# Kernel tuning notes

Hardware: AMD Instinct MI355X
Metric: run time of the kernel (lower is better)

The kernel has to match this reference:

```python
import jax, jax.numpy as jnp
import numpy as np

B, T, D = 2, 2048, 2048
H, KVH = 16, 4
HD = D // H            # 128
HALF = HD // 2         # 64
EPS = 1e-6


def zc_rmsnorm(x, scale):
    # zero-centred RMSNorm: (1+scale) * x / rms(x), rms in fp32
    rms = jnp.sqrt(jnp.mean(x.astype(jnp.float32) ** 2, axis=-1, keepdims=True) + EPS)
    return ((1.0 + scale) * x / rms).astype(x.dtype)


def apply_rope(x, cos, sin):
    # x: [B, h, T, HD]; cos/sin: [T, HALF]
    t = x.shape[2]
    c = cos[:t][None, None, :, :]
    s = sin[:t][None, None, :, :]
    x1, x2 = x[..., :HALF], x[..., HALF:]
    return jnp.concatenate([x1 * c - x2 * s, x2 * c + x1 * s], axis=-1)


def setup_inputs() -> dict:
    key = jax.random.key(0)
    ks = jax.random.split(key, 8)
    std = 0.02
    res_std = 0.02 / np.sqrt(2 * 24)
    q_input = jax.random.normal(ks[0], (B, T, D), jnp.float32)
    kv_input = jax.random.normal(ks[1], (B, T, D), jnp.float32)
    mask = jnp.tril(jnp.ones((T, T), bool))[None, None, :, :]
    inv_freq = 1.0 / (10000.0 ** (jnp.arange(0, HALF, dtype=jnp.float32) / HALF))
    ang = jnp.arange(T, dtype=jnp.float32)[:, None] * inv_freq[None, :]
    cos, sin = jnp.cos(ang), jnp.sin(ang)
    Wq = jax.random.normal(ks[2], (D, D), jnp.float32) * std
    Wk = jax.random.normal(ks[3], (D, KVH * HD), jnp.float32) * std
    Wv = jax.random.normal(ks[4], (D, KVH * HD), jnp.float32) * std
    q_scale = jnp.zeros((HD,), jnp.float32)
    k_scale = jnp.zeros((HD,), jnp.float32)
    Wo = jax.random.normal(ks[5], (D, D), jnp.float32) * res_std
    return {"q_input": q_input, "kv_input": kv_input, "mask": mask,
            "cos": cos, "sin": sin, "Wq": Wq, "Wk": Wk, "Wv": Wv,
            "q_scale": q_scale, "k_scale": k_scale, "Wo": Wo}


def reference(q_input, kv_input, mask, cos, sin, Wq, Wk, Wv, q_scale, k_scale, Wo):
    b = q_input.shape[0]
    q = (q_input @ Wq).reshape(b, -1, H, HD).transpose(0, 2, 1, 3)      # [B,H,T,HD]
    k = (kv_input @ Wk).reshape(b, -1, KVH, HD).transpose(0, 2, 1, 3)   # [B,KVH,T,HD]
    v = (kv_input @ Wv).reshape(b, -1, KVH, HD).transpose(0, 2, 1, 3)
    q = zc_rmsnorm(q, q_scale)
    k = zc_rmsnorm(k, k_scale)
    rep = H // KVH
    k = jnp.repeat(k, rep, axis=1)
    v = jnp.repeat(v, rep, axis=1)
    q = apply_rope(q, cos, sin)
    k = apply_rope(k, cos, sin)
    scale = jnp.sqrt(jnp.float32(HD))
    scores = jnp.einsum('bhqd,bhkd->bhqk', q, k) / scale                # [B,H,T,T]
    scores = jnp.where(mask, scores, jnp.finfo(scores.dtype).min)
    attn = jax.nn.softmax(scores, axis=-1)
    out = jnp.einsum('bhqk,bhkd->bhqd', attn, v)
    out = out.transpose(0, 2, 1, 3).reshape(b, -1, D)
    return out @ Wo
```

## Files before the change

kernel.cpp:

```cpp
#include <hip/hip_runtime.h>

#define NB 2
#define NT 2048
#define ND 2048
#define NH 16
#define NKVH 4
#define NHD 128
#define NHALF 64
#define NREP (NH / NKVH)
#define MFIX 12.0f

typedef __bf16 bf16x8 __attribute__((ext_vector_type(8)));
typedef unsigned short u16x8 __attribute__((ext_vector_type(8)));
typedef float f32x4 __attribute__((ext_vector_type(4)));

__device__ __forceinline__ unsigned short f2b(float f) {
  union { float f; unsigned int u; } v; v.f = f;
  unsigned int r = v.u + 0x7FFFu + ((v.u >> 16) & 1u);
  return (unsigned short)(r >> 16);
}
__device__ __forceinline__ float b2f(unsigned short h) {
  union { unsigned int u; float f; } v; v.u = ((unsigned int)h) << 16;
  return v.f;
}

__global__ __launch_bounds__(256) void f2bf(const float* __restrict__ in,
                                            unsigned short* __restrict__ out) {
  const size_t i = (size_t)(blockIdx.x * 256 + threadIdx.x) * 8;
  float4 a = *(const float4*)(in + i);
  float4 b = *(const float4*)(in + i + 4);
  u16x8 r;
  r[0] = f2b(a.x); r[1] = f2b(a.y); r[2] = f2b(a.z); r[3] = f2b(a.w);
  r[4] = f2b(b.x); r[5] = f2b(b.y); r[6] = f2b(b.z); r[7] = f2b(b.w);
  *(u16x8*)(out + i) = r;
}

__global__ __launch_bounds__(256) void wtrans(const float* __restrict__ in,
                                              unsigned short* __restrict__ out,
                                              int K, int N) {
  __shared__ float tile[32][33];
  const int k0 = blockIdx.y * 32, n0 = blockIdx.x * 32;
  const int x = threadIdx.x & 31, y8 = threadIdx.x >> 5;
#pragma unroll
  for (int j = 0; j < 4; ++j) {
    const int y = y8 + j * 8;
    tile[y][x] = in[(size_t)(k0 + y) * N + n0 + x];
  }
  __syncthreads();
#pragma unroll
  for (int j = 0; j < 4; ++j) {
    const int y = y8 + j * 8;
    out[(size_t)(n0 + y) * K + k0 + x] = f2b(tile[x][y]);
  }
}

__global__ __launch_bounds__(256) void gemm128(const unsigned short* __restrict__ A,
                                               const unsigned short* __restrict__ Bt,
                                               float* __restrict__ C,
                                               int M, int N, int K) {
  __shared__ unsigned short As[128 * 40];
  __shared__ unsigned short Bs[128 * 40];
  const int tid = threadIdx.x;
  const int wave = tid >> 6, lane = tid & 63;
  const int wm = wave >> 1, wn = wave & 1;
  const int quad = lane >> 4, c = lane & 15;
  const int m0 = blockIdx.y * 128, n0 = blockIdx.x * 128;
  const int sr = tid >> 2;
  const int sc = (tid & 3) * 8;

  f32x4 acc[4][4] = {};

  u16x8 a0 = *(const u16x8*)(A + (size_t)(m0 + sr) * K + sc);
  u16x8 a1 = *(const u16x8*)(A + (size_t)(m0 + 64 + sr) * K + sc);
  u16x8 b0 = *(const u16x8*)(Bt + (size_t)(n0 + sr) * K + sc);
  u16x8 b1 = *(const u16x8*)(Bt + (size_t)(n0 + 64 + sr) * K + sc);

  for (int k0 = 0; k0 < K; k0 += 32) {
    *(u16x8*)&As[sr * 40 + sc] = a0;
    *(u16x8*)&As[(64 + sr) * 40 + sc] = a1;
    *(u16x8*)&Bs[sr * 40 + sc] = b0;
    *(u16x8*)&Bs[(64 + sr) * 40 + sc] = b1;
    __syncthreads();
    const int kn = k0 + 32;
    if (kn < K) {
      a0 = *(const u16x8*)(A + (size_t)(m0 + sr) * K + kn + sc);
      a1 = *(const u16x8*)(A + (size_t)(m0 + 64 + sr) * K + kn + sc);
      b0 = *(const u16x8*)(Bt + (size_t)(n0 + sr) * K + kn + sc);
      b1 = *(const u16x8*)(Bt + (size_t)(n0 + 64 + sr) * K + kn + sc);
    }
    bf16x8 af[4];
#pragma unroll
    for (int sm = 0; sm < 4; ++sm)
      af[sm] = *(const bf16x8*)&As[(wm * 64 + sm * 16 + c) * 40 + quad * 8];
#pragma unroll
    for (int sn = 0; sn < 4; ++sn) {
      bf16x8 bfr = *(const bf16x8*)&Bs[(wn * 64 + sn * 16 + c) * 40 + quad * 8];
#pragma unroll
      for (int sm = 0; sm < 4; ++sm)
        acc[sm][sn] = __builtin_amdgcn_mfma_f32_16x16x32_bf16(af[sm], bfr, acc[sm][sn], 0, 0, 0);
    }
    __syncthreads();
  }

#pragma unroll
  for (int sm = 0; sm < 4; ++sm)
#pragma unroll
    for (int sn = 0; sn < 4; ++sn) {
      const int row = m0 + wm * 64 + sm * 16 + quad * 4;
      const int col = n0 + wn * 64 + sn * 16 + c;
#pragma unroll
      for (int r = 0; r < 4; ++r)
        C[(size_t)(row + r) * N + col] = acc[sm][sn][r];
    }
}

__global__ __launch_bounds__(256) void rmsnorm_rope(const float* __restrict__ in,
                                                    unsigned short* __restrict__ out,
                                                    const float* __restrict__ scale,
                                                    const float* __restrict__ cosp,
                                                    const float* __restrict__ sinp,
                                                    int nh, int instride, float outscale) {
  const int wid = blockIdx.x * 4 + (threadIdx.x >> 6);
  const int lane = threadIdx.x & 63;
  const int h = wid % nh;
  const int t = (wid / nh) % NT;
  const int b = wid / (nh * NT);
  const float* x = in + (size_t)(b * NT + t) * instride + h * NHD;
  float x1 = x[lane], x2 = x[lane + NHALF];
  float ss = x1 * x1 + x2 * x2;
#pragma unroll
  for (int m = 1; m < 64; m <<= 1) ss += __shfl_xor(ss, m, 64);
  const float inv = 1.0f / sqrtf(ss * (1.0f / NHD) + 1e-6f);
  const float n1 = (1.0f + scale[lane]) * x1 * inv;
  const float n2 = (1.0f + scale[lane + NHALF]) * x2 * inv;
  const float cc = cosp[t * NHALF + lane], s = sinp[t * NHALF + lane];
  const size_t ob = (((size_t)b * nh + h) * NT + t) * NHD;
  out[ob + lane] = f2b((n1 * cc - n2 * s) * outscale);
  out[ob + lane + NHALF] = f2b((n2 * cc + n1 * s) * outscale);
}

__global__ __launch_bounds__(256) void vtrans(const float* __restrict__ in,
                                              unsigned short* __restrict__ out,
                                              int instride) {
  __shared__ float tile[32][33];
  const int bg = blockIdx.z;
  const int b = bg >> 2, g = bg & 3;
  const int t0 = blockIdx.x * 32, d0 = blockIdx.y * 32;
  const int x = threadIdx.x & 31, y8 = threadIdx.x >> 5;
#pragma unroll
  for (int j = 0; j < 4; ++j) {
    const int y = y8 + j * 8;
    tile[y][x] = in[(size_t)(b * NT + t0 + y) * instride + g * NHD + d0 + x];
  }
  __syncthreads();
#pragma unroll
  for (int j = 0; j < 4; ++j) {
    const int y = y8 + j * 8;
    out[((size_t)bg * NHD + d0 + y) * NT + t0 + x] = f2b(tile[x][y]);
  }
}

__global__ __launch_bounds__(256, 3) void attn64(const unsigned short* __restrict__ Qh,
                                                 const unsigned short* __restrict__ Kh,
                                                 const unsigned short* __restrict__ Vtg,
                                                 unsigned short* __restrict__ O) {
  __shared__ unsigned short Kt[64 * 136];
  __shared__ unsigned short Vt[128 * 72];
  __shared__ unsigned short Pt[64 * 72];
  const int bh = blockIdx.x;
  const int b = bh / NH, h = bh % NH, g = h / NREP;
  const int y = blockIdx.y;
  const int a = y & 7, bb = y >> 3;
  const int qt = (bb == 0) ? a : (bb == 1) ? a + 8 : (bb == 2) ? 31 - a : 23 - a;
  const int tid = threadIdx.x;
  const int w = tid >> 6, lane = tid & 63;
  const int quad = lane >> 4, c = lane & 15;

  bf16x8 qf[4];
  {
    const unsigned short* qp =
        Qh + ((size_t)(b * NH + h) * NT + qt * 64 + w * 16 + c) * NHD + quad * 8;
#pragma unroll
    for (int ch = 0; ch < 4; ++ch) qf[ch] = *(const bf16x8*)(qp + ch * 32);
  }

  f32x4 acc_o[8] = {};
  float lsum[4] = {0.f, 0.f, 0.f, 0.f};
  const size_t kbase = (size_t)(b * NKVH + g) * NT * NHD;
  const size_t vbase = (size_t)(b * NKVH + g) * NHD * NT;
  const int nkt = qt + 1;

  for (int kt = 0; kt < nkt; ++kt) {
    const int k0 = kt * 64;
#pragma unroll
    for (int j = 0; j < 4; ++j) {
      const int f = j * 256 + tid;
      const int kr = f >> 4, kc_ = (f & 15) * 8;
      *(u16x8*)&Kt[kr * 136 + kc_] =
          *(const u16x8*)&Kh[kbase + (size_t)(k0 + kr) * NHD + kc_];
      const int vd = f >> 3, vc = (f & 7) * 8;
      *(u16x8*)&Vt[vd * 72 + vc] =
          *(const u16x8*)&Vtg[vbase + (size_t)vd * NT + k0 + vc];
    }
    __syncthreads();

    f32x4 s[4] = {};
#pragma unroll
    for (int n = 0; n < 4; ++n)
#pragma unroll
      for (int ch = 0; ch < 4; ++ch) {
        bf16x8 kf = *(const bf16x8*)&Kt[(n * 16 + c) * 136 + ch * 32 + quad * 8];
        s[n] = __builtin_amdgcn_mfma_f32_16x16x32_bf16(qf[ch], kf, s[n], 0, 0, 0);
      }

    const bool dmask = (kt == qt);
#pragma unroll
    for (int r = 0; r < 4; ++r) {
      float v0 = s[0][r], v1 = s[1][r], v2 = s[2][r], v3 = s[3][r];
      const int lrow = w * 16 + quad * 4 + r;
      if (dmask) {
        if (c > lrow) v0 = -1e30f;
        if (16 + c > lrow) v1 = -1e30f;
        if (32 + c > lrow) v2 = -1e30f;
        if (48 + c > lrow) v3 = -1e30f;
      }
      const float p0 = __expf(v0 - MFIX), p1 = __expf(v1 - MFIX);
      const float p2 = __expf(v2 - MFIX), p3 = __expf(v3 - MFIX);
      lsum[r] += (p0 + p1) + (p2 + p3);
      Pt[lrow * 72 + c] = f2b(p0);
      Pt[lrow * 72 + 16 + c] = f2b(p1);
      Pt[lrow * 72 + 32 + c] = f2b(p2);
      Pt[lrow * 72 + 48 + c] = f2b(p3);
    }

#pragma unroll
    for (int kc2 = 0; kc2 < 2; ++kc2) {
      bf16x8 pf = *(const bf16x8*)&Pt[(w * 16 + c) * 72 + kc2 * 32 + quad * 8];
#pragma unroll
      for (int n2 = 0; n2 < 8; ++n2) {
        bf16x8 vf = *(const bf16x8*)&Vt[(n2 * 16 + c) * 72 + kc2 * 32 + quad * 8];
        acc_o[n2] = __builtin_amdgcn_mfma_f32_16x16x32_bf16(pf, vf, acc_o[n2], 0, 0, 0);
      }
    }
    __syncthreads();
  }

#pragma unroll
  for (int r = 0; r < 4; ++r) {
    float l = lsum[r];
    l += __shfl_xor(l, 1, 64);
    l += __shfl_xor(l, 2, 64);
    l += __shfl_xor(l, 4, 64);
    l += __shfl_xor(l, 8, 64);
    lsum[r] = l;
  }

#pragma unroll
  for (int r = 0; r < 4; ++r) {
    const float invl = 1.0f / lsum[r];
    const int qrow = qt * 64 + w * 16 + quad * 4 + r;
    unsigned short* op = O + ((size_t)(b * NT + qrow) * NH + h) * NHD + c;
#pragma unroll
    for (int n2 = 0; n2 < 8; ++n2) op[n2 * 16] = f2b(acc_o[n2][r] * invl);
  }
}

extern "C" void kernel_launch(void* const* d_in, const int* in_sizes, int n_in,
                              void* d_out, int out_size, void* d_ws, size_t ws_size,
                              hipStream_t stream) {
  (void)in_sizes; (void)n_in; (void)out_size; (void)ws_size;
  const float* q_input  = (const float*)d_in[0];
  const float* kv_input = (const float*)d_in[1];
  const float* cosp = (const float*)d_in[3];
  const float* sinp = (const float*)d_in[4];
  const float* Wq = (const float*)d_in[5];
  const float* Wk = (const float*)d_in[6];
  const float* Wv = (const float*)d_in[7];
  const float* q_scale = (const float*)d_in[8];
  const float* k_scale = (const float*)d_in[9];
  const float* Wo = (const float*)d_in[10];
  float* out = (float*)d_out;

  char* p = (char*)d_ws;
  float* Q32  = (float*)p; p += (size_t)NB * NT * ND * 4;
  float* KVp  = (float*)p; p += (size_t)NB * NT * 1024 * 4;
  unsigned short* Qb16  = (unsigned short*)p; p += (size_t)NB * NT * ND * 2;
  unsigned short* KVb16 = (unsigned short*)p; p += (size_t)NB * NT * ND * 2;
  unsigned short* Kh  = (unsigned short*)p; p += (size_t)NB * NKVH * NT * NHD * 2;
  unsigned short* Vtg = (unsigned short*)p; p += (size_t)NB * NKVH * NT * NHD * 2;
  unsigned short* Wqt  = (unsigned short*)p; p += (size_t)ND * ND * 2;
  unsigned short* WkvT = (unsigned short*)p; p += (size_t)1024 * ND * 2;
  unsigned short* Wot  = (unsigned short*)p; p += (size_t)ND * ND * 2;
  unsigned short* Ob = Qb16;
  unsigned short* Qh = KVb16;

  const dim3 blk(256);
  const int M = NB * NT;

  f2bf<<<dim3(M * ND / 2048), blk, 0, stream>>>(q_input, Qb16);
  f2bf<<<dim3(M * ND / 2048), blk, 0, stream>>>(kv_input, KVb16);

  wtrans<<<dim3(ND / 32, ND / 32), blk, 0, stream>>>(Wq, Wqt, ND, ND);
  wtrans<<<dim3(512 / 32, ND / 32), blk, 0, stream>>>(Wk, WkvT, ND, 512);
  wtrans<<<dim3(512 / 32, ND / 32), blk, 0, stream>>>(Wv, WkvT + (size_t)512 * ND, ND, 512);
  wtrans<<<dim3(ND / 32, ND / 32), blk, 0, stream>>>(Wo, Wot, ND, ND);

  gemm128<<<dim3(ND / 128, M / 128), blk, 0, stream>>>(Qb16, Wqt, Q32, M, ND, ND);
  gemm128<<<dim3(1024 / 128, M / 128), blk, 0, stream>>>(KVb16, WkvT, KVp, M, 1024, ND);

  rmsnorm_rope<<<dim3(NB * NT * NH / 4), blk, 0, stream>>>(Q32, Qh, q_scale, cosp, sinp,
                                                           NH, ND, 0.08838834764831845f);
  rmsnorm_rope<<<dim3(NB * NT * NKVH / 4), blk, 0, stream>>>(KVp, Kh, k_scale, cosp, sinp,
                                                             NKVH, 1024, 1.0f);
  vtrans<<<dim3(NT / 32, NHD / 32, NB * NKVH), blk, 0, stream>>>(KVp + 512, Vtg, 1024);

  attn64<<<dim3(NB * NH, 32), blk, 0, stream>>>(Qh, Kh, Vtg, Ob);

  gemm128<<<dim3(ND / 128, M / 128), blk, 0, stream>>>(Ob, Wot, out, M, ND, ND);
}
```

Baseline: 426.0 us.

## Use direct global-to-LDS loads in GEMM and register-prefetch K/V in attention

The GEMM drops its register-staged prefetch and instead copies tiles straight from global memory into unpadded LDS with global_load_lds. The attention kernel adds a software pipeline: the next K/V tile is loaded into registers while the current tile is being computed. LDS row padding also changes in attention (136→132, 72→68). In exchange, the GEMM loses its load/compute overlap and its padding, so LDS bank conflicts may rise. The new attention strides also break 16-byte alignment of the vector LDS accesses.

```diff
diff --git a/kernel.cpp b/kernel.cpp
--- a/kernel.cpp
+++ b/kernel.cpp
@@ -24,6 +24,13 @@
   return v.f;
 }
 
+__device__ __forceinline__ void glds16(const unsigned short* g, unsigned short* l) {
+  __builtin_amdgcn_global_load_lds(
+      (__attribute__((address_space(1))) unsigned int*)(unsigned long long)g,
+      (__attribute__((address_space(3))) unsigned int*)(unsigned int)(unsigned long long)l,
+      16, 0, 0);
+}
+
 __global__ __launch_bounds__(256) void f2bf(const float* __restrict__ in,
                                             unsigned short* __restrict__ out) {
   const size_t i = (size_t)(blockIdx.x * 256 + threadIdx.x) * 8;
@@ -58,43 +65,40 @@
                                                const unsigned short* __restrict__ Bt,
                                                float* __restrict__ C,
                                                int M, int N, int K) {
-  __shared__ unsigned short As[128 * 40];
-  __shared__ unsigned short Bs[128 * 40];
+  __shared__ unsigned short As[128 * 32];
+  __shared__ unsigned short Bs[128 * 32];
   const int tid = threadIdx.x;
   const int wave = tid >> 6, lane = tid & 63;
   const int wm = wave >> 1, wn = wave & 1;
   const int quad = lane >> 4, c = lane & 15;
   const int m0 = blockIdx.y * 128, n0 = blockIdx.x * 128;
-  const int sr = tid >> 2;
-  const int sc = (tid & 3) * 8;
+  const int gr = lane >> 2;
+  const int gc = (lane & 3) * 8;
+
+  const unsigned short* pa0 = A + (size_t)(m0 + wave * 16 + gr) * K + gc;
+  const unsigned short* pa1 = A + (size_t)(m0 + 64 + wave * 16 + gr) * K + gc;
+  const unsigned short* pb0 = Bt + (size_t)(n0 + wave * 16 + gr) * K + gc;
+  const unsigned short* pb1 = Bt + (size_t)(n0 + 64 + wave * 16 + gr) * K + gc;
+  unsigned short* la0 = &As[(wave * 16) * 32];
+  unsigned short* la1 = &As[(64 + wave * 16) * 32];
+  unsigned short* lb0 = &Bs[(wave * 16) * 32];
+  unsigned short* lb1 = &Bs[(64 + wave * 16) * 32];
 
   f32x4 acc[4][4] = {};
 
-  u16x8 a0 = *(const u16x8*)(A + (size_t)(m0 + sr) * K + sc);
-  u16x8 a1 = *(const u16x8*)(A + (size_t)(m0 + 64 + sr) * K + sc);
-  u16x8 b0 = *(const u16x8*)(Bt + (size_t)(n0 + sr) * K + sc);
-  u16x8 b1 = *(const u16x8*)(Bt + (size_t)(n0 + 64 + sr) * K + sc);
-
   for (int k0 = 0; k0 < K; k0 += 32) {
-    *(u16x8*)&As[sr * 40 + sc] = a0;
-    *(u16x8*)&As[(64 + sr) * 40 + sc] = a1;
-    *(u16x8*)&Bs[sr * 40 + sc] = b0;
-    *(u16x8*)&Bs[(64 + sr) * 40 + sc] = b1;
+    glds16(pa0 + k0, la0);
+    glds16(pa1 + k0, la1);
+    glds16(pb0 + k0, lb0);
+    glds16(pb1 + k0, lb1);
     __syncthreads();
-    const int kn = k0 + 32;
-    if (kn < K) {
-      a0 = *(const u16x8*)(A + (size_t)(m0 + sr) * K + kn + sc);
-      a1 = *(const u16x8*)(A + (size_t)(m0 + 64 + sr) * K + kn + sc);
-      b0 = *(const u16x8*)(Bt + (size_t)(n0 + sr) * K + kn + sc);
-      b1 = *(const u16x8*)(Bt + (size_t)(n0 + 64 + sr) * K + kn + sc);
-    }
     bf16x8 af[4];
 #pragma unroll
     for (int sm = 0; sm < 4; ++sm)
-      af[sm] = *(const bf16x8*)&As[(wm * 64 + sm * 16 + c) * 40 + quad * 8];
+      af[sm] = *(const bf16x8*)&As[(wm * 64 + sm * 16 + c) * 32 + quad * 8];
 #pragma unroll
     for (int sn = 0; sn < 4; ++sn) {
-      bf16x8 bfr = *(const bf16x8*)&Bs[(wn * 64 + sn * 16 + c) * 40 + quad * 8];
+      bf16x8 bfr = *(const bf16x8*)&Bs[(wn * 64 + sn * 16 + c) * 32 + quad * 8];
 #pragma unroll
       for (int sm = 0; sm < 4; ++sm)
         acc[sm][sn] = __builtin_amdgcn_mfma_f32_16x16x32_bf16(af[sm], bfr, acc[sm][sn], 0, 0, 0);
@@ -164,9 +168,9 @@
                                                  const unsigned short* __restrict__ Kh,
                                                  const unsigned short* __restrict__ Vtg,
                                                  unsigned short* __restrict__ O) {
-  __shared__ unsigned short Kt[64 * 136];
-  __shared__ unsigned short Vt[128 * 72];
-  __shared__ unsigned short Pt[64 * 72];
+  __shared__ unsigned short Kt[64 * 132];
+  __shared__ unsigned short Vt[128 * 68];
+  __shared__ unsigned short Pt[64 * 68];
   const int bh = blockIdx.x;
   const int b = bh / NH, h = bh % NH, g = h / NREP;
   const int y = blockIdx.y;
@@ -190,26 +194,39 @@
   const size_t vbase = (size_t)(b * NKVH + g) * NHD * NT;
   const int nkt = qt + 1;
 
+  u16x8 kreg[4], vreg[4];
+#pragma unroll
+  for (int j = 0; j < 4; ++j) {
+    const int f = j * 256 + tid;
+    kreg[j] = *(const u16x8*)&Kh[kbase + (size_t)(f >> 4) * NHD + (f & 15) * 8];
+    vreg[j] = *(const u16x8*)&Vtg[vbase + (size_t)(f >> 3) * NT + (f & 7) * 8];
+  }
+
   for (int kt = 0; kt < nkt; ++kt) {
-    const int k0 = kt * 64;
 #pragma unroll
     for (int j = 0; j < 4; ++j) {
       const int f = j * 256 + tid;
-      const int kr = f >> 4, kc_ = (f & 15) * 8;
-      *(u16x8*)&Kt[kr * 136 + kc_] =
-          *(const u16x8*)&Kh[kbase + (size_t)(k0 + kr) * NHD + kc_];
-      const int vd = f >> 3, vc = (f & 7) * 8;
-      *(u16x8*)&Vt[vd * 72 + vc] =
-          *(const u16x8*)&Vtg[vbase + (size_t)vd * NT + k0 + vc];
+      *(u16x8*)&Kt[(f >> 4) * 132 + (f & 15) * 8] = kreg[j];
+      *(u16x8*)&Vt[(f >> 3) * 68 + (f & 7) * 8] = vreg[j];
     }
     __syncthreads();
 
+    if (kt + 1 < nkt) {
+      const int k0 = (kt + 1) * 64;
+#pragma unroll
+      for (int j = 0; j < 4; ++j) {
+        const int f = j * 256 + tid;
+        kreg[j] = *(const u16x8*)&Kh[kbase + (size_t)(k0 + (f >> 4)) * NHD + (f & 15) * 8];
+        vreg[j] = *(const u16x8*)&Vtg[vbase + (size_t)(f >> 3) * NT + k0 + (f & 7) * 8];
+      }
+    }
+
     f32x4 s[4] = {};
 #pragma unroll
     for (int n = 0; n < 4; ++n)
 #pragma unroll
       for (int ch = 0; ch < 4; ++ch) {
-        bf16x8 kf = *(const bf16x8*)&Kt[(n * 16 + c) * 136 + ch * 32 + quad * 8];
+        bf16x8 kf = *(const bf16x8*)&Kt[(n * 16 + c) * 132 + ch * 32 + quad * 8];
         s[n] = __builtin_amdgcn_mfma_f32_16x16x32_bf16(qf[ch], kf, s[n], 0, 0, 0);
       }
 
@@ -227,18 +244,18 @@
       const float p0 = __expf(v0 - MFIX), p1 = __expf(v1 - MFIX);
       const float p2 = __expf(v2 - MFIX), p3 = __expf(v3 - MFIX);
       lsum[r] += (p0 + p1) + (p2 + p3);
-      Pt[lrow * 72 + c] = f2b(p0);
-      Pt[lrow * 72 + 16 + c] = f2b(p1);
-      Pt[lrow * 72 + 32 + c] = f2b(p2);
-      Pt[lrow * 72 + 48 + c] = f2b(p3);
+      Pt[lrow * 68 + c] = f2b(p0);
+      Pt[lrow * 68 + 16 + c] = f2b(p1);
+      Pt[lrow * 68 + 32 + c] = f2b(p2);
+      Pt[lrow * 68 + 48 + c] = f2b(p3);
     }
 
 #pragma unroll
     for (int kc2 = 0; kc2 < 2; ++kc2) {
-      bf16x8 pf = *(const bf16x8*)&Pt[(w * 16 + c) * 72 + kc2 * 32 + quad * 8];
+      bf16x8 pf = *(const bf16x8*)&Pt[(w * 16 + c) * 68 + kc2 * 32 + quad * 8];
 #pragma unroll
       for (int n2 = 0; n2 < 8; ++n2) {
-        bf16x8 vf = *(const bf16x8*)&Vt[(n2 * 16 + c) * 72 + kc2 * 32 + quad * 8];
+        bf16x8 vf = *(const bf16x8*)&Vt[(n2 * 16 + c) * 68 + kc2 * 32 + quad * 8];
         acc_o[n2] = __builtin_amdgcn_mfma_f32_16x16x32_bf16(pf, vf, acc_o[n2], 0, 0, 0);
       }
     }
```

Result: no change. 426.3 us (+0.1%).
